# Optimization experiments

Measured on AMD Instinct MI355X. Metric: run time of the kernel, lower is better.

Reference implementation:

```python
import jax, jax.numpy as jnp
import numpy as np

N_NODES = 100000
N_EDGES = 1600000
IN_DIM = 128
HEADS = 4
HEAD_DIM = 16  # hidden_dim 64 // 4 heads
HID = HEADS * HEAD_DIM
NEG_SLOPE = 0.2


def setup_inputs() -> dict:
    key = jax.random.key(0)
    ks = jax.random.split(key, 20)
    inp = {
        "x": jax.random.normal(ks[0], (N_NODES, IN_DIM), dtype=jnp.float32),
        "edge_index": jax.random.randint(ks[1], (2, N_EDGES), 0, N_NODES, dtype=jnp.int32),
    }
    dims = [IN_DIM, HID, HID]
    for l in range(3):
        d_in = dims[l]
        sc = 1.0 / np.sqrt(d_in)
        inp[f"w{l}"] = jax.random.normal(ks[2 + 4 * l], (d_in, HID), dtype=jnp.float32) * sc
        inp[f"asrc{l}"] = jax.random.normal(ks[3 + 4 * l], (HEADS, HEAD_DIM), dtype=jnp.float32) * 0.1
        inp[f"adst{l}"] = jax.random.normal(ks[4 + 4 * l], (HEADS, HEAD_DIM), dtype=jnp.float32) * 0.1
        inp[f"b{l}"] = jnp.zeros((HID,), dtype=jnp.float32)
    inp["out_w"] = jax.random.normal(ks[14], (HID, 1), dtype=jnp.float32) * (1.0 / np.sqrt(HID))
    inp["out_b"] = jnp.zeros((1,), dtype=jnp.float32)
    return inp


def _gat_layer(h, src, dst, W, a_src, a_dst, b):
    # h: [N, d_in]; src/dst: [E'] (self-loops already appended)
    n = h.shape[0]
    xh = (h @ W).reshape(n, HEADS, HEAD_DIM)              # [N,H,C]
    al_s = jnp.sum(xh * a_src, axis=-1)                   # [N,H]
    al_d = jnp.sum(xh * a_dst, axis=-1)                   # [N,H]
    e = jax.nn.leaky_relu(al_s[src] + al_d[dst], NEG_SLOPE)  # [E',H]
    # segment-softmax over incoming edges of each destination node
    m = jax.ops.segment_max(e, dst, num_segments=n)       # [N,H]
    p = jnp.exp(e - m[dst])
    z = jax.ops.segment_sum(p, dst, num_segments=n)       # [N,H]
    alpha = p / (z[dst] + 1e-16)                          # [E',H]
    msg = xh[src] * alpha[:, :, None]                     # [E',H,C]
    out = jax.ops.segment_sum(msg, dst, num_segments=n)   # [N,H,C]
    return out.reshape(n, HID) + b


def reference(x, edge_index, w0, asrc0, adst0, b0, w1, asrc1, adst1, b1,
              w2, asrc2, adst2, b2, out_w, out_b):
    n = x.shape[0]
    loops = jnp.arange(n, dtype=edge_index.dtype)
    src = jnp.concatenate([edge_index[0], loops])  # PyG GATConv adds self-loops
    dst = jnp.concatenate([edge_index[1], loops])
    h = x
    params = [(w0, asrc0, adst0, b0), (w1, asrc1, adst1, b1), (w2, asrc2, adst2, b2)]
    for W, a_s, a_d, b in params:
        h = _gat_layer(h, src, dst, W, a_s, a_d, b)
        h = jax.nn.relu(h)
    return (h @ out_w + out_b).squeeze(-1)  # [N]
```

## Files before the change

### kernel.cpp

```cpp
#include <hip/hip_runtime.h>


#define NBMAX 512
#define SCHUNK 4096
#define BCAP 8192
#define PADSLACK 768

typedef __attribute__((ext_vector_type(8))) short bf16x8;
typedef __attribute__((ext_vector_type(4))) float f32x4;
typedef _Float16 half_t;

__device__ inline unsigned short bf16_rtn(float x) {
    union { float f; unsigned u; } a; a.f = x;
    return (unsigned short)((a.u + 0x7FFFu + ((a.u >> 16) & 1u)) >> 16);
}
__device__ inline float bf16_to_f(unsigned short s) {
    union { unsigned u; float f; } b; b.u = ((unsigned)s) << 16;
    return b.f;
}

__global__ __launch_bounds__(256) void k_prep(const float* __restrict__ w0, const float* __restrict__ w1,
                                              const float* __restrict__ w2,
                                              unsigned short* __restrict__ p0h, unsigned short* __restrict__ p0l,
                                              unsigned short* __restrict__ p1h, unsigned short* __restrict__ p1l,
                                              unsigned short* __restrict__ p2h, unsigned short* __restrict__ p2l,
                                              int* __restrict__ bhist, float* __restrict__ als,
                                              half_t* __restrict__ xh16, int n) {
    int bid = blockIdx.x, t = threadIdx.x;
    if (bid == 8) {
        bhist[t] = 0;
        bhist[t + 256] = 0;
        if (t < 4) als[(size_t)n * 4 + t] = -1e30f;
        if (t < 64) xh16[(size_t)n * 64 + t] = (half_t)0.f;
        return;
    }
    int g = bid * 256 + t;
    const float* W;
    unsigned short *ph, *pl;
    int idx;
    if (g < 1024) { W = w0; ph = p0h; pl = p0l; idx = g; }
    else if (g < 1536) { W = w1; ph = p1h; pl = p1l; idx = g - 1024; }
    else if (g < 2048) { W = w2; ph = p2h; pl = p2l; idx = g - 1536; }
    else return;
    int ko = idx >> 6, nn = idx & 63;
#pragma unroll
    for (int j = 0; j < 8; ++j) {
        float w = W[(size_t)(ko * 8 + j) * 64 + nn];
        unsigned short hb = bf16_rtn(w);
        ph[(size_t)idx * 8 + j] = hb;
        pl[(size_t)idx * 8 + j] = bf16_rtn(w - bf16_to_f(hb));
    }
}

__global__ __launch_bounds__(256) void k_bhist(const int* __restrict__ dst, int* __restrict__ bhist, int e) {
    __shared__ unsigned int h[NBMAX];
    int t = threadIdx.x;
    h[t] = 0;
    h[t + 256] = 0;
    __syncthreads();
    for (int i = blockIdx.x * 256 + t; i < e; i += gridDim.x * 256)
        atomicAdd(&h[dst[i] >> 8], 1u);
    __syncthreads();
    if (h[t]) atomicAdd(&bhist[t], (int)h[t]);
    if (h[t + 256]) atomicAdd(&bhist[t + 256], (int)h[t + 256]);
}

__global__ __launch_bounds__(512) void k_bscan(const int* __restrict__ bhist, int* __restrict__ boffs,
                                               int* __restrict__ bfill, int nb, int e) {
    __shared__ int s[NBMAX];
    int t = threadIdx.x;
    int v = (t < nb) ? bhist[t] : 0;
    s[t] = v;
    __syncthreads();
    for (int o = 1; o < 512; o <<= 1) {
        int add = (t >= o) ? s[t - o] : 0;
        __syncthreads();
        s[t] += add;
        __syncthreads();
    }
    boffs[t] = s[t] - v;
    if (t == 511) boffs[512] = s[511];
    bfill[t] = 0;
}

template <int D_IN>
__device__ __forceinline__ void mgemm_wave(const float* __restrict__ h,
                                           const unsigned short* __restrict__ wph,
                                           const unsigned short* __restrict__ wpl,
                                           const float* __restrict__ asrc, const float* __restrict__ adst,
                                           float* __restrict__ xh, half_t* __restrict__ xh16,
                                           float* __restrict__ als,
                                           float* __restrict__ ald, float* __restrict__ mvec,
                                           int m0, int lane, int n) {
    int quad = lane >> 4, l16 = lane & 15;
    int node_a = m0 + l16;
    int mm = min(node_a, n - 1);
    const float* hrow = h + (size_t)mm * D_IN + quad * 8;

    f32x4 acc[4];
#pragma unroll
    for (int i = 0; i < 4; ++i) acc[i] = (f32x4){0.f, 0.f, 0.f, 0.f};

    constexpr int KSTEPS = D_IN / 32;
#pragma unroll
    for (int s = 0; s < KSTEPS; ++s) {
        float4 a0 = *(const float4*)(hrow + s * 32);
        float4 a1 = *(const float4*)(hrow + s * 32 + 4);
        float av[8] = {a0.x, a0.y, a0.z, a0.w, a1.x, a1.y, a1.z, a1.w};
        bf16x8 ahi, alo;
#pragma unroll
        for (int j = 0; j < 8; ++j) {
            unsigned short hb = bf16_rtn(av[j]);
            ahi[j] = (short)hb;
            alo[j] = (short)bf16_rtn(av[j] - bf16_to_f(hb));
        }
        const unsigned short* bbase = wph + ((size_t)((s * 4 + quad) * 64 + l16)) * 8;
        const unsigned short* bbasel = wpl + ((size_t)((s * 4 + quad) * 64 + l16)) * 8;
#pragma unroll
        for (int nt = 0; nt < 4; ++nt) {
            bf16x8 bhi = *(const bf16x8*)(bbase + (size_t)nt * 16 * 8);
            bf16x8 blo = *(const bf16x8*)(bbasel + (size_t)nt * 16 * 8);
            acc[nt] = __builtin_amdgcn_mfma_f32_16x16x32_bf16(ahi, bhi, acc[nt], 0, 0, 0);
            acc[nt] = __builtin_amdgcn_mfma_f32_16x16x32_bf16(ahi, blo, acc[nt], 0, 0, 0);
            acc[nt] = __builtin_amdgcn_mfma_f32_16x16x32_bf16(alo, bhi, acc[nt], 0, 0, 0);
        }
    }
#pragma unroll
    for (int nt = 0; nt < 4; ++nt) {
        float as_l = asrc[nt * 16 + l16];
        float ad_l = adst[nt * 16 + l16];
#pragma unroll
        for (int r = 0; r < 4; ++r) {
            int node = m0 + quad * 4 + r;
            float c = acc[nt][r];
            if (node < n) {
                xh[(size_t)node * 64 + nt * 16 + l16] = c;
                xh16[(size_t)node * 64 + nt * 16 + l16] = (half_t)c;
            }
            float ps = c * as_l, pd = c * ad_l;
            ps += __shfl_xor(ps, 1, 64); pd += __shfl_xor(pd, 1, 64);
            ps += __shfl_xor(ps, 2, 64); pd += __shfl_xor(pd, 2, 64);
            ps += __shfl_xor(ps, 4, 64); pd += __shfl_xor(pd, 4, 64);
            ps += __shfl_xor(ps, 8, 64); pd += __shfl_xor(pd, 8, 64);
            if (l16 == 0 && node < n) {
                als[node * 4 + nt] = ps;
                ald[node * 4 + nt] = pd;
                float sm = ps + pd;
                mvec[node * 4 + nt] = sm >= 0.f ? sm : 0.2f * sm;
            }
        }
    }
}

template <int D_IN>
__global__ __launch_bounds__(256) void k_mgemm(const float* __restrict__ h,
                                               const unsigned short* __restrict__ wph,
                                               const unsigned short* __restrict__ wpl,
                                               const float* __restrict__ asrc, const float* __restrict__ adst,
                                               float* __restrict__ xh, half_t* __restrict__ xh16,
                                               float* __restrict__ als,
                                               float* __restrict__ ald, float* __restrict__ mvec, int n) {
    int t = threadIdx.x;
    int m0 = blockIdx.x * 64 + (t >> 6) * 16;
    mgemm_wave<D_IN>(h, wph, wpl, asrc, adst, xh, xh16, als, ald, mvec, m0, t & 63, n);
}

__global__ __launch_bounds__(512) void k_mix1(const int* __restrict__ src, const int* __restrict__ dst,
                                              const int* __restrict__ boffs, int* __restrict__ bfill,
                                              unsigned int* __restrict__ edata, int e, int sb,
                                              const float* __restrict__ x,
                                              const unsigned short* __restrict__ p0h,
                                              const unsigned short* __restrict__ p0l,
                                              const float* __restrict__ asrc, const float* __restrict__ adst,
                                              float* __restrict__ xh, half_t* __restrict__ xh16,
                                              float* __restrict__ als,
                                              float* __restrict__ ald, float* __restrict__ mvec, int n) {
    __shared__ unsigned int hist[NBMAX];
    __shared__ unsigned int loc[NBMAX];
    __shared__ int gbase[NBMAX];
    __shared__ unsigned int stmp[NBMAX];
    __shared__ unsigned int sortbuf[SCHUNK];
    __shared__ int posbuf[SCHUNK];
    int t = threadIdx.x;
    if (blockIdx.x >= sb) {
        int mblk = blockIdx.x - sb;
        int m0 = mblk * 128 + (t >> 6) * 16;
        mgemm_wave<128>(x, p0h, p0l, asrc, adst, xh, xh16, als, ald, mvec, m0, t & 63, n);
        return;
    }
    int i0 = blockIdx.x * SCHUNK;
    int cnt = min(SCHUNK, e - i0);
    hist[t] = 0;
    __syncthreads();
    for (int j = t; j < cnt; j += 512) atomicAdd(&hist[dst[i0 + j] >> 8], 1u);
    __syncthreads();
    unsigned int v = hist[t];
    stmp[t] = v;
    __syncthreads();
    for (int o = 1; o < 512; o <<= 1) {
        unsigned int add = (t >= o) ? stmp[t - o] : 0;
        __syncthreads();
        stmp[t] += add;
        __syncthreads();
    }
    loc[t] = stmp[t] - v;
    int gb = 0;
    if (v > 0) gb = atomicAdd(&bfill[t], (int)v);
    gbase[t] = boffs[t] + gb - (int)loc[t];
    hist[t] = loc[t];
    __syncthreads();
    for (int j = t; j < cnt; j += 512) {
        int d = dst[i0 + j];
        int s = src[i0 + j];
        int b = d >> 8;
        unsigned int p = atomicAdd(&hist[b], 1u);
        sortbuf[p] = (unsigned int)s | ((unsigned int)(d & 255) << 24);
        posbuf[p] = gbase[b] + (int)p;
    }
    __syncthreads();
    for (int j = t; j < cnt; j += 512) edata[posbuf[j]] = sortbuf[j];
}

__global__ __launch_bounds__(512) void k_mix2(const unsigned int* __restrict__ edata,
                                              const int* __restrict__ boffs, int* __restrict__ poffs,
                                              int* __restrict__ pend, int* __restrict__ ssrc,
                                              int n, int nb, int mg1,
                                              const float* __restrict__ x,
                                              const unsigned short* __restrict__ p0h,
                                              const unsigned short* __restrict__ p0l,
                                              const float* __restrict__ asrc, const float* __restrict__ adst,
                                              float* __restrict__ xh, half_t* __restrict__ xh16,
                                              float* __restrict__ als,
                                              float* __restrict__ ald, float* __restrict__ mvec) {
    __shared__ unsigned int hist[256];
    __shared__ unsigned int stmp[256];
    __shared__ unsigned int loc2[256];
    __shared__ unsigned int srcbuf[BCAP];
    int t = threadIdx.x;
    if (blockIdx.x >= nb) {
        int mblk = mg1 + (blockIdx.x - nb);
        int m0 = mblk * 128 + (t >> 6) * 16;
        mgemm_wave<128>(x, p0h, p0l, asrc, adst, xh, xh16, als, ald, mvec, m0, t & 63, n);
        return;
    }
    int b = blockIdx.x;
    int e0 = boffs[b], e1 = boffs[b + 1];
    int cnt = e1 - e0;
    int pb = e0 + b * PADSLACK;
    if (t < 256) hist[t] = 0;
    __syncthreads();
    for (int j = t; j < cnt; j += 512) atomicAdd(&hist[edata[e0 + j] >> 24], 1u);
    __syncthreads();
    unsigned int v = 0, v4 = 0;
    if (t < 256) {
        v = hist[t];
        v4 = (v + 3u) & ~3u;
        stmp[t] = v4;
    }
    __syncthreads();
    for (int o = 1; o < 256; o <<= 1) {
        unsigned int add = 0;
        if (t < 256 && t >= o) add = stmp[t - o];
        __syncthreads();
        if (t < 256) stmp[t] += add;
        __syncthreads();
    }
    int ptot = (int)stmp[255];
    if (t < 256) {
        loc2[t] = stmp[t] - v4;
        int node = b * 256 + t;
        if (node < n) {
            poffs[node] = pb + (int)loc2[t];
            pend[node] = pb + (int)(loc2[t] + v4);
        }
        hist[t] = loc2[t];
    }
    __syncthreads();
    if (cnt + PADSLACK <= BCAP) {
        for (int j = t; j < cnt; j += 512) {
            unsigned int p = edata[e0 + j];
            unsigned int pos = atomicAdd(&hist[p >> 24], 1u);
            srcbuf[pos] = p & 0xFFFFFFu;
        }
        if (t < 256)
            for (unsigned int k = v; k < v4; ++k) srcbuf[loc2[t] + k] = (unsigned int)n;
        __syncthreads();
        for (int j = t; j < ptot; j += 512) ssrc[pb + j] = (int)srcbuf[j];
    } else {
        for (int j = t; j < cnt; j += 512) {
            unsigned int p = edata[e0 + j];
            unsigned int pos = atomicAdd(&hist[p >> 24], 1u);
            ssrc[pb + (int)pos] = (int)(p & 0xFFFFFFu);
        }
        if (t < 256)
            for (unsigned int k = v; k < v4; ++k) ssrc[pb + (int)(loc2[t] + k)] = n;
    }
}

__device__ inline float4 lrelu4(float4 v) {
    float4 r;
    r.x = v.x >= 0.f ? v.x : 0.2f * v.x;
    r.y = v.y >= 0.f ? v.y : 0.2f * v.y;
    r.z = v.z >= 0.f ? v.z : 0.2f * v.z;
    r.w = v.w >= 0.f ? v.w : 0.2f * v.w;
    return r;
}

#define ACCUM(LO, HI, ACCA, ACCB, ZS)                                           \
    {                                                                           \
        int g_ = ((LO) - s0) >> 2, gb_ = ((HI) - s0) >> 2;                      \
        for (; g_ + 4 <= gb_; g_ += 4) {                                        \
            int4 uu0 = *(const int4*)&ub[g_ * 4];                               \
            int4 uu1 = *(const int4*)&ub[g_ * 4 + 4];                           \
            int4 uu2 = *(const int4*)&ub[g_ * 4 + 8];                           \
            int4 uu3 = *(const int4*)&ub[g_ * 4 + 12];                          \
            float4 pp0 = *(const float4*)&per[g_ * 4];                          \
            float4 pp1 = *(const float4*)&per[g_ * 4 + 4];                      \
            float4 pp2 = *(const float4*)&per[g_ * 4 + 8];                      \
            float4 pp3 = *(const float4*)&per[g_ * 4 + 12];                     \
            float x0 = (float)*(const half_t*)(xl + (size_t)(unsigned)uu0.x);   \
            float x1 = (float)*(const half_t*)(xl + (size_t)(unsigned)uu0.y);   \
            float x2 = (float)*(const half_t*)(xl + (size_t)(unsigned)uu0.z);   \
            float x3 = (float)*(const half_t*)(xl + (size_t)(unsigned)uu0.w);   \
            float x4 = (float)*(const half_t*)(xl + (size_t)(unsigned)uu1.x);   \
            float x5 = (float)*(const half_t*)(xl + (size_t)(unsigned)uu1.y);   \
            float x6 = (float)*(const half_t*)(xl + (size_t)(unsigned)uu1.z);   \
            float x7 = (float)*(const half_t*)(xl + (size_t)(unsigned)uu1.w);   \
            float x8 = (float)*(const half_t*)(xl + (size_t)(unsigned)uu2.x);   \
            float x9 = (float)*(const half_t*)(xl + (size_t)(unsigned)uu2.y);   \
            float xa = (float)*(const half_t*)(xl + (size_t)(unsigned)uu2.z);   \
            float xb = (float)*(const half_t*)(xl + (size_t)(unsigned)uu2.w);   \
            float xc = (float)*(const half_t*)(xl + (size_t)(unsigned)uu3.x);   \
            float xd = (float)*(const half_t*)(xl + (size_t)(unsigned)uu3.y);   \
            float xe = (float)*(const half_t*)(xl + (size_t)(unsigned)uu3.z);   \
            float xf = (float)*(const half_t*)(xl + (size_t)(unsigned)uu3.w);   \
            ZS += pp0.x + pp0.y + pp0.z + pp0.w;                                \
            ZS += pp1.x + pp1.y + pp1.z + pp1.w;                                \
            ZS += pp2.x + pp2.y + pp2.z + pp2.w;                                \
            ZS += pp3.x + pp3.y + pp3.z + pp3.w;                                \
            ACCA += pp0.x * x0; ACCB += pp0.y * x1;                             \
            ACCA += pp0.z * x2; ACCB += pp0.w * x3;                             \
            ACCA += pp1.x * x4; ACCB += pp1.y * x5;                             \
            ACCA += pp1.z * x6; ACCB += pp1.w * x7;                             \
            ACCA += pp2.x * x8; ACCB += pp2.y * x9;                             \
            ACCA += pp2.z * xa; ACCB += pp2.w * xb;                             \
            ACCA += pp3.x * xc; ACCB += pp3.y * xd;                             \
            ACCA += pp3.z * xe; ACCB += pp3.w * xf;                             \
        }                                                                       \
        for (; g_ < gb_; ++g_) {                                                \
            int4 uu = *(const int4*)&ub[g_ * 4];                                \
            float4 pp = *(const float4*)&per[g_ * 4];                           \
            float x0 = (float)*(const half_t*)(xl + (size_t)(unsigned)uu.x);    \
            float x1 = (float)*(const half_t*)(xl + (size_t)(unsigned)uu.y);    \
            float x2 = (float)*(const half_t*)(xl + (size_t)(unsigned)uu.z);    \
            float x3 = (float)*(const half_t*)(xl + (size_t)(unsigned)uu.w);    \
            ZS += pp.x + pp.y + pp.z + pp.w;                                    \
            ACCA += pp.x * x0; ACCB += pp.y * x1;                               \
            ACCA += pp.z * x2; ACCB += pp.w * x3;                               \
        }                                                                       \
    }

__global__ __launch_bounds__(256) void k_agg(const float* __restrict__ xh,
                                             const half_t* __restrict__ xh16,
                                             const float* __restrict__ als, const float* __restrict__ ald,
                                             const float* __restrict__ mvec,
                                             const int* __restrict__ poffs, const int* __restrict__ pend,
                                             const int* __restrict__ ssrc,
                                             const float* __restrict__ bias, float* __restrict__ hout,
                                             const float* __restrict__ outw, const float* __restrict__ outb,
                                             float* __restrict__ fout, int n) {
    __shared__ int s_u[4][64];
    __shared__ float s_pe[4][4][64];
    int wslot = threadIdx.x >> 6;
    int lane = threadIdx.x & 63;
    int w = (blockIdx.x * 256 + threadIdx.x) >> 6;
    int v0 = w << 2;
    if (v0 >= n) return;
    int head = lane >> 4;
    int* ub = s_u[wslot];
    float* per = s_pe[wslot][head];
    float* pew = &s_pe[wslot][0][lane];

    int vlast = n - 1;
    int last = min(v0 + 3, vlast);
    int4 rr = *(const int4*)(poffs + v0);
    int e3 = pend[last];
    int r0 = rr.x;
    int r1 = (v0 + 1 <= last) ? rr.y : e3;
    int r2 = (v0 + 2 <= last) ? rr.z : e3;
    int r3 = (v0 + 3 <= last) ? rr.w : e3;

    const char* xl = (const char*)(xh16 + lane);
    float acc0a = xh[((size_t)(unsigned)v0 << 6) + lane];
    float acc1a = xh[((size_t)(unsigned)min(v0 + 1, vlast) << 6) + lane];
    float acc2a = xh[((size_t)(unsigned)min(v0 + 2, vlast) << 6) + lane];
    float acc3a = xh[((size_t)(unsigned)min(v0 + 3, vlast) << 6) + lane];
    float acc0b = 0.f, acc1b = 0.f, acc2b = 0.f, acc3b = 0.f;
    float zs0 = 0.f, zs1 = 0.f, zs2 = 0.f, zs3 = 0.f;

    int s0 = r0;
    int u_n = n;
    if (s0 < e3) {
        if (lane < e3 - s0) u_n = ssrc[s0 + lane];
    }
    float4 alu_n = *(const float4*)(als + 4 * (size_t)u_n);
    int e_n = s0 + lane;
    int nid_n = min(v0 + (e_n >= r1) + (e_n >= r2) + (e_n >= r3), vlast);
    float4 ald_n = *(const float4*)(ald + 4 * (size_t)nid_n);
    float4 m_n = *(const float4*)(mvec + 4 * (size_t)nid_n);

    while (s0 < e3) {
        int cnt = min(64, e3 - s0);
        float4 e4 = lrelu4(make_float4(alu_n.x + ald_n.x, alu_n.y + ald_n.y,
                                       alu_n.z + ald_n.z, alu_n.w + ald_n.w));
        float4 pe;
        pe.x = __expf(e4.x - m_n.x);
        pe.y = __expf(e4.y - m_n.y);
        pe.z = __expf(e4.z - m_n.z);
        pe.w = __expf(e4.w - m_n.w);
        ub[lane] = u_n << 7;
        pew[0] = pe.x;
        pew[64] = pe.y;
        pew[128] = pe.z;
        pew[192] = pe.w;
        int s1 = s0 + 64;
        if (s1 < e3) {
            u_n = n;
            if (lane < e3 - s1) u_n = ssrc[s1 + lane];
            alu_n = *(const float4*)(als + 4 * (size_t)u_n);
            int e1 = s1 + lane;
            int nid1 = min(v0 + (e1 >= r1) + (e1 >= r2) + (e1 >= r3), vlast);
            ald_n = *(const float4*)(ald + 4 * (size_t)nid1);
            m_n = *(const float4*)(mvec + 4 * (size_t)nid1);
        }
        int lim = s0 + cnt;
        int hi0 = min(r1, lim);
        int lo1 = max(r1, s0), hi1 = min(r2, lim);
        int lo2 = max(r2, s0), hi2 = min(r3, lim);
        int lo3 = max(r3, s0);
        ACCUM(s0, hi0, acc0a, acc0b, zs0);
        ACCUM(lo1, hi1, acc1a, acc1b, zs1);
        ACCUM(lo2, hi2, acc2a, acc2b, zs2);
        ACCUM(lo3, lim, acc3a, acc3b, zs3);
        s0 = s1;
    }

    float bl = bias[lane];
    float o0 = fmaxf((acc0a + acc0b) / (1.f + zs0 + 1e-16f) + bl, 0.f);
    float o1 = fmaxf((acc1a + acc1b) / (1.f + zs1 + 1e-16f) + bl, 0.f);
    float o2 = fmaxf((acc2a + acc2b) / (1.f + zs2 + 1e-16f) + bl, 0.f);
    float o3 = fmaxf((acc3a + acc3b) / (1.f + zs3 + 1e-16f) + bl, 0.f);
    if (outw) {
        float ow = outw[lane];
        float ob = outb[0];
        float t0 = o0 * ow, t1 = o1 * ow, t2 = o2 * ow, t3 = o3 * ow;
#pragma unroll
        for (int d = 32; d; d >>= 1) {
            t0 += __shfl_down(t0, d, 64);
            t1 += __shfl_down(t1, d, 64);
            t2 += __shfl_down(t2, d, 64);
            t3 += __shfl_down(t3, d, 64);
        }
        if (lane == 0) {
            fout[v0] = t0 + ob;
            if (v0 + 1 < n) fout[v0 + 1] = t1 + ob;
            if (v0 + 2 < n) fout[v0 + 2] = t2 + ob;
            if (v0 + 3 < n) fout[v0 + 3] = t3 + ob;
        }
    } else {
        hout[((size_t)v0 << 6) + lane] = o0;
        if (v0 + 1 < n) hout[((size_t)(v0 + 1) << 6) + lane] = o1;
        if (v0 + 2 < n) hout[((size_t)(v0 + 2) << 6) + lane] = o2;
        if (v0 + 3 < n) hout[((size_t)(v0 + 3) << 6) + lane] = o3;
    }
}

extern "C" void kernel_launch(void* const* d_in, const int* in_sizes, int n_in,
                              void* d_out, int out_size, void* d_ws, size_t ws_size,
                              hipStream_t stream) {
    const float* x = (const float*)d_in[0];
    const int* ei = (const int*)d_in[1];
    const float* w[3] = {(const float*)d_in[2], (const float*)d_in[6], (const float*)d_in[10]};
    const float* as[3] = {(const float*)d_in[3], (const float*)d_in[7], (const float*)d_in[11]};
    const float* ad[3] = {(const float*)d_in[4], (const float*)d_in[8], (const float*)d_in[12]};
    const float* b[3] = {(const float*)d_in[5], (const float*)d_in[9], (const float*)d_in[13]};
    const float* outw = (const float*)d_in[14];
    const float* outb = (const float*)d_in[15];

    const int N = in_sizes[0] / 128;
    const int E = in_sizes[1] / 2;
    const int* src = ei;
    const int* dst = ei + E;
    const int NB = (N + 255) / 256;
    const int SB = (E + SCHUNK - 1) / SCHUNK;
    const int GB128 = (N + 127) / 128;
    const int MG1 = (GB128 + 1) / 2;
    const int MG2 = GB128 - MG1;

    char* ws = (char*)d_ws;
    auto alloc = [&](size_t bytes) -> void* {
        void* p = (void*)ws;
        ws += (bytes + 255) & ~(size_t)255;
        return p;
    };
    int* bhist = (int*)alloc(NBMAX * 4);
    int* boffs = (int*)alloc((NBMAX + 1) * 4);
    int* bfill = (int*)alloc(NBMAX * 4);
    int* poffs = (int*)alloc((size_t)(N + 8) * 4);
    int* pend = (int*)alloc((size_t)N * 4);
    int* ssrc = (int*)alloc((size_t)(E + NBMAX * PADSLACK + 256) * 4);
    unsigned int* edata = (unsigned int*)alloc((size_t)(E + 64) * 4);
    float* xh = (float*)alloc((size_t)N * 64 * 4);
    half_t* xh16 = (half_t*)alloc((size_t)(N + 1) * 64 * 2);
    float* hbuf = (float*)alloc((size_t)N * 64 * 4);
    float* als = (float*)alloc((size_t)(N + 1) * 4 * 4);
    float* ald = (float*)alloc((size_t)N * 4 * 4);
    float* mvec = (float*)alloc((size_t)N * 4 * 4);
    unsigned short* p0h = (unsigned short*)alloc(8192 * 2);
    unsigned short* p0l = (unsigned short*)alloc(8192 * 2);
    unsigned short* p1h = (unsigned short*)alloc(4096 * 2);
    unsigned short* p1l = (unsigned short*)alloc(4096 * 2);
    unsigned short* p2h = (unsigned short*)alloc(4096 * 2);
    unsigned short* p2l = (unsigned short*)alloc(4096 * 2);

    k_prep<<<9, 256, 0, stream>>>(w[0], w[1], w[2], p0h, p0l, p1h, p1l, p2h, p2l, bhist, als, xh16, N);
    k_bhist<<<256, 256, 0, stream>>>(dst, bhist, E);
    k_bscan<<<1, 512, 0, stream>>>(bhist, boffs, bfill, NB, E);
    k_mix1<<<SB + MG1, 512, 0, stream>>>(src, dst, boffs, bfill, edata, E, SB,
                                         x, p0h, p0l, as[0], ad[0], xh, xh16, als, ald, mvec, N);
    k_mix2<<<NB + MG2, 512, 0, stream>>>(edata, boffs, poffs, pend, ssrc, N, NB, MG1,
                                         x, p0h, p0l, as[0], ad[0], xh, xh16, als, ald, mvec);

    const int gblocks = (N + 63) / 64;
    const int ablocks = (N + 15) / 16;

    k_agg<<<ablocks, 256, 0, stream>>>(xh, xh16, als, ald, mvec, poffs, pend, ssrc, b[0], hbuf, nullptr, nullptr, nullptr, N);
    k_mgemm<64><<<gblocks, 256, 0, stream>>>(hbuf, p1h, p1l, as[1], ad[1], xh, xh16, als, ald, mvec, N);
    k_agg<<<ablocks, 256, 0, stream>>>(xh, xh16, als, ald, mvec, poffs, pend, ssrc, b[1], hbuf, nullptr, nullptr, nullptr, N);
    k_mgemm<64><<<gblocks, 256, 0, stream>>>(hbuf, p2h, p2l, as[2], ad[2], xh, xh16, als, ald, mvec, N);
    k_agg<<<ablocks, 256, 0, stream>>>(xh, xh16, als, ald, mvec, poffs, pend, ssrc, b[2], nullptr, outw, outb, (float*)d_out, N);
}
```

Baseline: 375.9 us.

## Store hidden activations in fp16, drop fp32 xh copy, fuse bucket histogram into prep

Removes the fp32 xh buffer: the aggregation now reads the self-loop term from the fp16 xh16 array, and the intermediate layer outputs (hbuf) are stored in fp16. The 64-wide GEMM reads fp16 input through a new template path. The bucket histogram kernel is merged into k_prep as extra blocks, bhist is zeroed with a memset, and edata now shares storage with hbuf. This cuts memory traffic and one launch, but lowers the precision of the intermediate activations and the self-loop term.

Result: faster. 362.0 us, median of 2 (-3.7%).

```diff
diff --git a/kernel.cpp b/kernel.cpp
--- a/kernel.cpp
+++ b/kernel.cpp
@@ -5,10 +5,12 @@
 #define SCHUNK 4096
 #define BCAP 8192
 #define PADSLACK 768
+#define NBH 256
 
 typedef __attribute__((ext_vector_type(8))) short bf16x8;
 typedef __attribute__((ext_vector_type(4))) float f32x4;
 typedef _Float16 half_t;
+typedef __attribute__((ext_vector_type(8))) _Float16 half8;
 
 __device__ inline unsigned short bf16_rtn(float x) {
     union { float f; unsigned u; } a; a.f = x;
@@ -24,14 +26,25 @@
                                               unsigned short* __restrict__ p0h, unsigned short* __restrict__ p0l,
                                               unsigned short* __restrict__ p1h, unsigned short* __restrict__ p1l,
                                               unsigned short* __restrict__ p2h, unsigned short* __restrict__ p2l,
-                                              int* __restrict__ bhist, float* __restrict__ als,
-                                              half_t* __restrict__ xh16, int n) {
+                                              int* __restrict__ bhist, const int* __restrict__ dst, int e,
+                                              float* __restrict__ als, half_t* __restrict__ xh16, int n) {
+    __shared__ unsigned int h[NBMAX];
     int bid = blockIdx.x, t = threadIdx.x;
     if (bid == 8) {
-        bhist[t] = 0;
-        bhist[t + 256] = 0;
         if (t < 4) als[(size_t)n * 4 + t] = -1e30f;
         if (t < 64) xh16[(size_t)n * 64 + t] = (half_t)0.f;
+        return;
+    }
+    if (bid >= 9) {
+        int bb = bid - 9;
+        h[t] = 0;
+        h[t + 256] = 0;
+        __syncthreads();
+        for (int i = bb * 256 + t; i < e; i += NBH * 256)
+            atomicAdd(&h[dst[i] >> 8], 1u);
+        __syncthreads();
+        if (h[t]) atomicAdd(&bhist[t], (int)h[t]);
+        if (h[t + 256]) atomicAdd(&bhist[t + 256], (int)h[t + 256]);
         return;
     }
     int g = bid * 256 + t;
@@ -52,19 +65,6 @@
     }
 }
 
-__global__ __launch_bounds__(256) void k_bhist(const int* __restrict__ dst, int* __restrict__ bhist, int e) {
-    __shared__ unsigned int h[NBMAX];
-    int t = threadIdx.x;
-    h[t] = 0;
-    h[t + 256] = 0;
-    __syncthreads();
-    for (int i = blockIdx.x * 256 + t; i < e; i += gridDim.x * 256)
-        atomicAdd(&h[dst[i] >> 8], 1u);
-    __syncthreads();
-    if (h[t]) atomicAdd(&bhist[t], (int)h[t]);
-    if (h[t + 256]) atomicAdd(&bhist[t + 256], (int)h[t + 256]);
-}
-
 __global__ __launch_bounds__(512) void k_bscan(const int* __restrict__ bhist, int* __restrict__ boffs,
                                                int* __restrict__ bfill, int nb, int e) {
     __shared__ int s[NBMAX];
@@ -83,19 +83,17 @@
     bfill[t] = 0;
 }
 
-template <int D_IN>
-__device__ __forceinline__ void mgemm_wave(const float* __restrict__ h,
+template <int D_IN, bool HALF_IN>
+__device__ __forceinline__ void mgemm_wave(const void* __restrict__ hv,
                                            const unsigned short* __restrict__ wph,
                                            const unsigned short* __restrict__ wpl,
                                            const float* __restrict__ asrc, const float* __restrict__ adst,
-                                           float* __restrict__ xh, half_t* __restrict__ xh16,
-                                           float* __restrict__ als,
+                                           half_t* __restrict__ xh16, float* __restrict__ als,
                                            float* __restrict__ ald, float* __restrict__ mvec,
                                            int m0, int lane, int n) {
     int quad = lane >> 4, l16 = lane & 15;
     int node_a = m0 + l16;
     int mm = min(node_a, n - 1);
-    const float* hrow = h + (size_t)mm * D_IN + quad * 8;
 
     f32x4 acc[4];
 #pragma unroll
@@ -104,9 +102,19 @@
     constexpr int KSTEPS = D_IN / 32;
 #pragma unroll
     for (int s = 0; s < KSTEPS; ++s) {
-        float4 a0 = *(const float4*)(hrow + s * 32);
-        float4 a1 = *(const float4*)(hrow + s * 32 + 4);
-        float av[8] = {a0.x, a0.y, a0.z, a0.w, a1.x, a1.y, a1.z, a1.w};
+        float av[8];
+        if constexpr (HALF_IN) {
+            const half_t* hrow = (const half_t*)hv + (size_t)mm * D_IN + quad * 8;
+            half8 hvv = *(const half8*)(hrow + s * 32);
+#pragma unroll
+            for (int j = 0; j < 8; ++j) av[j] = (float)hvv[j];
+        } else {
+            const float* hrow = (const float*)hv + (size_t)mm * D_IN + quad * 8;
+            float4 a0 = *(const float4*)(hrow + s * 32);
+            float4 a1 = *(const float4*)(hrow + s * 32 + 4);
+            av[0] = a0.x; av[1] = a0.y; av[2] = a0.z; av[3] = a0.w;
+            av[4] = a1.x; av[5] = a1.y; av[6] = a1.z; av[7] = a1.w;
+        }
         bf16x8 ahi, alo;
 #pragma unroll
         for (int j = 0; j < 8; ++j) {
@@ -133,10 +141,7 @@
         for (int r = 0; r < 4; ++r) {
             int node = m0 + quad * 4 + r;
             float c = acc[nt][r];
-            if (node < n) {
-                xh[(size_t)node * 64 + nt * 16 + l16] = c;
-                xh16[(size_t)node * 64 + nt * 16 + l16] = (half_t)c;
-            }
+            if (node < n) xh16[(size_t)node * 64 + nt * 16 + l16] = (half_t)c;
             float ps = c * as_l, pd = c * ad_l;
             ps += __shfl_xor(ps, 1, 64); pd += __shfl_xor(pd, 1, 64);
             ps += __shfl_xor(ps, 2, 64); pd += __shfl_xor(pd, 2, 64);
@@ -152,17 +157,15 @@
     }
 }
 
-template <int D_IN>
-__global__ __launch_bounds__(256) void k_mgemm(const float* __restrict__ h,
-                                               const unsigned short* __restrict__ wph,
-                                               const unsigned short* __restrict__ wpl,
-                                               const float* __restrict__ asrc, const float* __restrict__ adst,
-                                               float* __restrict__ xh, half_t* __restrict__ xh16,
-                                               float* __restrict__ als,
-                                               float* __restrict__ ald, float* __restrict__ mvec, int n) {
+__global__ __launch_bounds__(256) void k_mgemm64(const half_t* __restrict__ h,
+                                                 const unsigned short* __restrict__ wph,
+                                                 const unsigned short* __restrict__ wpl,
+                                                 const float* __restrict__ asrc, const float* __restrict__ adst,
+                                                 half_t* __restrict__ xh16, float* __restrict__ als,
+                                                 float* __restrict__ ald, float* __restrict__ mvec, int n) {
     int t = threadIdx.x;
     int m0 = blockIdx.x * 64 + (t >> 6) * 16;
-    mgemm_wave<D_IN>(h, wph, wpl, asrc, adst, xh, xh16, als, ald, mvec, m0, t & 63, n);
+    mgemm_wave<64, true>(h, wph, wpl, asrc, adst, xh16, als, ald, mvec, m0, t & 63, n);
 }
 
 __global__ __launch_bounds__(512) void k_mix1(const int* __restrict__ src, const int* __restrict__ dst,
@@ -172,8 +175,7 @@
                                               const unsigned short* __restrict__ p0h,
                                               const unsigned short* __restrict__ p0l,
                                               const float* __restrict__ asrc, const float* __restrict__ adst,
-                                              float* __restrict__ xh, half_t* __restrict__ xh16,
-                                              float* __restrict__ als,
+                                              half_t* __restrict__ xh16, float* __restrict__ als,
                                               float* __restrict__ ald, float* __restrict__ mvec, int n) {
     __shared__ unsigned int hist[NBMAX];
     __shared__ unsigned int loc[NBMAX];
@@ -185,7 +187,7 @@
     if (blockIdx.x >= sb) {
         int mblk = blockIdx.x - sb;
         int m0 = mblk * 128 + (t >> 6) * 16;
-        mgemm_wave<128>(x, p0h, p0l, asrc, adst, xh, xh16, als, ald, mvec, m0, t & 63, n);
+        mgemm_wave<128, false>(x, p0h, p0l, asrc, adst, xh16, als, ald, mvec, m0, t & 63, n);
         return;
     }
     int i0 = blockIdx.x * SCHUNK;
@@ -229,8 +231,7 @@
                                               const unsigned short* __restrict__ p0h,
                                               const unsigned short* __restrict__ p0l,
                                               const float* __restrict__ asrc, const float* __restrict__ adst,
-                                              float* __restrict__ xh, half_t* __restrict__ xh16,
-                                              float* __restrict__ als,
+                                              half_t* __restrict__ xh16, float* __restrict__ als,
                                               float* __restrict__ ald, float* __restrict__ mvec) {
     __shared__ unsigned int hist[256];
     __shared__ unsigned int stmp[256];
@@ -240,7 +241,7 @@
     if (blockIdx.x >= nb) {
         int mblk = mg1 + (blockIdx.x - nb);
         int m0 = mblk * 128 + (t >> 6) * 16;
-        mgemm_wave<128>(x, p0h, p0l, asrc, adst, xh, xh16, als, ald, mvec, m0, t & 63, n);
+        mgemm_wave<128, false>(x, p0h, p0l, asrc, adst, xh16, als, ald, mvec, m0, t & 63, n);
         return;
     }
     int b = blockIdx.x;
@@ -360,13 +361,12 @@
         }                                                                       \
     }
 
-__global__ __launch_bounds__(256) void k_agg(const float* __restrict__ xh,
-                                             const half_t* __restrict__ xh16,
+__global__ __launch_bounds__(256) void k_agg(const half_t* __restrict__ xh16,
                                              const float* __restrict__ als, const float* __restrict__ ald,
                                              const float* __restrict__ mvec,
                                              const int* __restrict__ poffs, const int* __restrict__ pend,
                                              const int* __restrict__ ssrc,
-                                             const float* __restrict__ bias, float* __restrict__ hout,
+                                             const float* __restrict__ bias, half_t* __restrict__ hout,
                                              const float* __restrict__ outw, const float* __restrict__ outb,
                                              float* __restrict__ fout, int n) {
     __shared__ int s_u[4][64];
@@ -391,10 +391,10 @@
     int r3 = (v0 + 3 <= last) ? rr.w : e3;
 
     const char* xl = (const char*)(xh16 + lane);
-    float acc0a = xh[((size_t)(unsigned)v0 << 6) + lane];
-    float acc1a = xh[((size_t)(unsigned)min(v0 + 1, vlast) << 6) + lane];
-    float acc2a = xh[((size_t)(unsigned)min(v0 + 2, vlast) << 6) + lane];
-    float acc3a = xh[((size_t)(unsigned)min(v0 + 3, vlast) << 6) + lane];
+    float acc0a = (float)xh16[((size_t)(unsigned)v0 << 6) + lane];
+    float acc1a = (float)xh16[((size_t)(unsigned)min(v0 + 1, vlast) << 6) + lane];
+    float acc2a = (float)xh16[((size_t)(unsigned)min(v0 + 2, vlast) << 6) + lane];
+    float acc3a = (float)xh16[((size_t)(unsigned)min(v0 + 3, vlast) << 6) + lane];
     float acc0b = 0.f, acc1b = 0.f, acc2b = 0.f, acc3b = 0.f;
     float zs0 = 0.f, zs1 = 0.f, zs2 = 0.f, zs3 = 0.f;
 
@@ -468,10 +468,10 @@
             if (v0 + 3 < n) fout[v0 + 3] = t3 + ob;
         }
     } else {
-        hout[((size_t)v0 << 6) + lane] = o0;
-        if (v0 + 1 < n) hout[((size_t)(v0 + 1) << 6) + lane] = o1;
-        if (v0 + 2 < n) hout[((size_t)(v0 + 2) << 6) + lane] = o2;
-        if (v0 + 3 < n) hout[((size_t)(v0 + 3) << 6) + lane] = o3;
+        hout[((size_t)v0 << 6) + lane] = (half_t)o0;
+        if (v0 + 1 < n) hout[((size_t)(v0 + 1) << 6) + lane] = (half_t)o1;
+        if (v0 + 2 < n) hout[((size_t)(v0 + 2) << 6) + lane] = (half_t)o2;
+        if (v0 + 3 < n) hout[((size_t)(v0 + 3) << 6) + lane] = (half_t)o3;
     }
 }
 
@@ -509,10 +509,8 @@
     int* poffs = (int*)alloc((size_t)(N + 8) * 4);
     int* pend = (int*)alloc((size_t)N * 4);
     int* ssrc = (int*)alloc((size_t)(E + NBMAX * PADSLACK + 256) * 4);
-    unsigned int* edata = (unsigned int*)alloc((size_t)(E + 64) * 4);
-    float* xh = (float*)alloc((size_t)N * 64 * 4);
     half_t* xh16 = (half_t*)alloc((size_t)(N + 1) * 64 * 2);
-    float* hbuf = (float*)alloc((size_t)N * 64 * 4);
+    half_t* hbuf = (half_t*)alloc((size_t)N * 64 * 2);
     float* als = (float*)alloc((size_t)(N + 1) * 4 * 4);
     float* ald = (float*)alloc((size_t)N * 4 * 4);
     float* mvec = (float*)alloc((size_t)N * 4 * 4);
@@ -522,21 +520,23 @@
     unsigned short* p1l = (unsigned short*)alloc(4096 * 2);
     unsigned short* p2h = (unsigned short*)alloc(4096 * 2);
     unsigned short* p2l = (unsigned short*)alloc(4096 * 2);
-
-    k_prep<<<9, 256, 0, stream>>>(w[0], w[1], w[2], p0h, p0l, p1h, p1l, p2h, p2l, bhist, als, xh16, N);
-    k_bhist<<<256, 256, 0, stream>>>(dst, bhist, E);
+    unsigned int* edata = (unsigned int*)hbuf;
+
+    hipMemsetAsync(bhist, 0, NBMAX * 4, stream);
+    k_prep<<<9 + NBH, 256, 0, stream>>>(w[0], w[1], w[2], p0h, p0l, p1h, p1l, p2h, p2l,
+                                        bhist, dst, E, als, xh16, N);
     k_bscan<<<1, 512, 0, stream>>>(bhist, boffs, bfill, NB, E);
     k_mix1<<<SB + MG1, 512, 0, stream>>>(src, dst, boffs, bfill, edata, E, SB,
-                                         x, p0h, p0l, as[0], ad[0], xh, xh16, als, ald, mvec, N);
+                                         x, p0h, p0l, as[0], ad[0], xh16, als, ald, mvec, N);
     k_mix2<<<NB + MG2, 512, 0, stream>>>(edata, boffs, poffs, pend, ssrc, N, NB, MG1,
-                                         x, p0h, p0l, as[0], ad[0], xh, xh16, als, ald, mvec);
+                                         x, p0h, p0l, as[0], ad[0], xh16, als, ald, mvec);
 
     const int gblocks = (N + 63) / 64;
     const int ablocks = (N + 15) / 16;
 
-    k_agg<<<ablocks, 256, 0, stream>>>(xh, xh16, als, ald, mvec, poffs, pend, ssrc, b[0], hbuf, nullptr, nullptr, nullptr, N);
-    k_mgemm<64><<<gblocks, 256, 0, stream>>>(hbuf, p1h, p1l, as[1], ad[1], xh, xh16, als, ald, mvec, N);
-    k_agg<<<ablocks, 256, 0, stream>>>(xh, xh16, als, ald, mvec, poffs, pend, ssrc, b[1], hbuf, nullptr, nullptr, nullptr, N);
-    k_mgemm<64><<<gblocks, 256, 0, stream>>>(hbuf, p2h, p2l, as[2], ad[2], xh, xh16, als, ald, mvec, N);
-    k_agg<<<ablocks, 256, 0, stream>>>(xh, xh16, als, ald, mvec, poffs, pend, ssrc, b[2], nullptr, outw, outb, (float*)d_out, N);
-}
+    k_agg<<<ablocks, 256, 0, stream>>>(xh16, als, ald, mvec, poffs, pend, ssrc, b[0], hbuf, nullptr, nullptr, nullptr, N);
+    k_mgemm64<<<gblocks, 256, 0, stream>>>(hbuf, p1h, p1l, as[1], ad[1], xh16, als, ald, mvec, N);
+    k_agg<<<ablocks, 256, 0, stream>>>(xh16, als, ald, mvec, poffs, pend, ssrc, b[1], hbuf, nullptr, nullptr, nullptr, N);
+    k_mgemm64<<<gblocks, 256, 0, stream>>>(hbuf, p2h, p2l, as[2], ad[2], xh16, als, ald, mvec, N);
+    k_agg<<<ablocks, 256, 0, stream>>>(xh16, als, ald, mvec, poffs, pend, ssrc, b[2], nullptr, outw, outb, (float*)d_out, N);
+}
```
